# Performance work log

Hardware: AMD Instinct MI355X
Metric: run time of the kernel (lower is better)

The kernel has to match this reference:

```python
import jax, jax.numpy as jnp
import numpy as np

TAU = 0.7        # init kwarg tau
BIG_NEG = -1.0e9 # matches torch big_neg
B, R = 8192, 4096


def setup_inputs() -> dict:
    key = jax.random.key(0)
    k1, k2 = jax.random.split(key)
    s = jax.random.normal(k1, (B, R), dtype=jnp.float32)
    mask = jax.random.uniform(k2, (B, R), dtype=jnp.float32)  # compared against 0.5
    return {"s": s, "mask": mask, "k": 8}


def reference(s, mask, k):
    # mask-apply then temperature scale
    z = jnp.where(mask > 0.5, s, jnp.full_like(s, BIG_NEG)) / max(TAU, 1e-6)
    # sparsemax along axis 1: sort descending, cumsum, support-size threshold
    z_sorted = -jnp.sort(-z, axis=1)                       # [B, R] descending
    z_cumsum = jnp.cumsum(z_sorted, axis=1)                # [B, R]
    r = jnp.arange(1, R + 1, dtype=z.dtype)[None, :]       # [1, R] ranks 1..R
    cond = 1.0 + r * z_sorted > z_cumsum                   # [B, R] support indicator
    k_sup = jnp.sum(cond, axis=1, keepdims=True)           # [B, 1] int support size
    tau_star = (jnp.take_along_axis(z_cumsum, k_sup - 1, axis=1) - 1.0) / k_sup.astype(z.dtype)
    p = jnp.maximum(z - tau_star, 0.0)                     # sparsemax probs, sum=1
    # scale by budget k and clip to [0, 1]
    return jnp.minimum(jnp.asarray(float(k), z.dtype) * p, 1.0)
```

## Files before the change

### kernel.cpp

```cpp
#include <hip/hip_runtime.h>


#define R_DIM 4096
#define BLOCK 256
#define V4T   4
#define BIG_NEG -1.0e9f
#define INV_TAU (1.0f / 0.7f)

typedef float fx4 __attribute__((ext_vector_type(4)));

__global__ __launch_bounds__(BLOCK, 4)
void gate_sparsemax_k_kernel(const float* __restrict__ s,
                             const float* __restrict__ m,
                             const int*  __restrict__ kptr,
                             float* __restrict__ out)
{
    __shared__ float red_sum[2][4];
    __shared__ float red_cnt[2][4];
    __shared__ float red_max[4];

    const int tid  = (int)threadIdx.x;
    const int lane = tid & 63;
    const int wid  = tid >> 6;
    const int row  = (int)blockIdx.x;

    const float kf = (float)(*kptr);

    const size_t base = (size_t)row * R_DIM;
    const fx4* sv4 = (const fx4*)(s + base);
    const fx4* mv4 = (const fx4*)(m + base);
    fx4*       ov4 = (fx4*)(out + base);

    fx4 sv[V4T], mv[V4T];
    #pragma unroll
    for (int t = 0; t < V4T; ++t) sv[t] = __builtin_nontemporal_load(&sv4[t * BLOCK + tid]);
    #pragma unroll
    for (int t = 0; t < V4T; ++t) mv[t] = __builtin_nontemporal_load(&mv4[t * BLOCK + tid]);
    __builtin_amdgcn_sched_barrier(0);

    fx4 zz[V4T];
    float zmax = -3.4028235e38f;
    #pragma unroll
    for (int t = 0; t < V4T; ++t) {
        fx4 zv;
        zv.x = (mv[t].x > 0.5f ? sv[t].x : BIG_NEG) * INV_TAU;
        zv.y = (mv[t].y > 0.5f ? sv[t].y : BIG_NEG) * INV_TAU;
        zv.z = (mv[t].z > 0.5f ? sv[t].z : BIG_NEG) * INV_TAU;
        zv.w = (mv[t].w > 0.5f ? sv[t].w : BIG_NEG) * INV_TAU;
        zz[t] = zv;
        zmax = fmaxf(zmax, fmaxf(fmaxf(zv.x, zv.y), fmaxf(zv.z, zv.w)));
    }

    #pragma unroll
    for (int off = 32; off >= 1; off >>= 1)
        zmax = fmaxf(zmax, __shfl_xor(zmax, off, 64));
    if (lane == 0) red_max[wid] = zmax;
    __syncthreads();
    zmax = fmaxf(fmaxf(red_max[0], red_max[1]), fmaxf(red_max[2], red_max[3]));

    float tau = zmax - 1.0f;
    for (int it = 0; it < 50; ++it) {
        float ssum = 0.0f, cnt = 0.0f;
        #pragma unroll
        for (int t = 0; t < V4T; ++t) {
            const fx4 zv = zz[t];
            if (zv.x > tau) { ssum += zv.x; cnt += 1.0f; }
            if (zv.y > tau) { ssum += zv.y; cnt += 1.0f; }
            if (zv.z > tau) { ssum += zv.z; cnt += 1.0f; }
            if (zv.w > tau) { ssum += zv.w; cnt += 1.0f; }
        }
        #pragma unroll
        for (int off = 32; off >= 1; off >>= 1) {
            ssum += __shfl_xor(ssum, off, 64);
            cnt  += __shfl_xor(cnt,  off, 64);
        }
        const int p = it & 1;
        if (lane == 0) { red_sum[p][wid] = ssum; red_cnt[p][wid] = cnt; }
        __syncthreads();
        const float S = ((red_sum[p][0] + red_sum[p][1]) + (red_sum[p][2] + red_sum[p][3]));
        const float C = ((red_cnt[p][0] + red_cnt[p][1]) + (red_cnt[p][2] + red_cnt[p][3]));
        const float tnew = (S - 1.0f) / C;
        if (tnew == tau) break;
        tau = tnew;
    }

    #pragma unroll
    for (int t = 0; t < V4T; ++t) {
        const fx4 zv = zz[t];
        fx4 ov;
        ov.x = fminf(kf * fmaxf(zv.x - tau, 0.0f), 1.0f);
        ov.y = fminf(kf * fmaxf(zv.y - tau, 0.0f), 1.0f);
        ov.z = fminf(kf * fmaxf(zv.z - tau, 0.0f), 1.0f);
        ov.w = fminf(kf * fmaxf(zv.w - tau, 0.0f), 1.0f);
        __builtin_nontemporal_store(ov, &ov4[t * BLOCK + tid]);
    }
}

extern "C" void kernel_launch(void* const* d_in, const int* in_sizes, int n_in,
                              void* d_out, int out_size, void* d_ws, size_t ws_size,
                              hipStream_t stream) {
    const float* s = (const float*)d_in[0];
    const float* m = (const float*)d_in[1];
    const int*   k = (const int*)d_in[2];
    float* out = (float*)d_out;

    const int nrows = in_sizes[0] / R_DIM;
    gate_sparsemax_k_kernel<<<nrows, BLOCK, 0, stream>>>(s, m, k, out);
}
```

Measured before the change: 291.4 us.

## Map one row per wavefront to drop block-level barriers in sparsemax iteration

Each 64-lane wavefront now owns a whole row of 4096 elements (16 float4 per lane) instead of a 256-thread block sharing a row, so the max and the per-iteration sum reductions need only wave shuffles, with no shared memory or __syncthreads. The support count is taken with ballot+popcount instead of a float shuffle reduction, and mask loads are split into two halves to limit register pressure. In exchange, register use per thread rises sharply (64 floats of z plus mask staging), which can lower occupancy under the launch bounds and reduce memory-level parallelism in this bandwidth-bound kernel.

```diff
diff --git a/kernel.cpp b/kernel.cpp
--- a/kernel.cpp
+++ b/kernel.cpp
@@ -3,26 +3,34 @@
 
 #define R_DIM 4096
 #define BLOCK 256
-#define V4T   4
+#define RPB   4
+#define NCH   16
 #define BIG_NEG -1.0e9f
 #define INV_TAU (1.0f / 0.7f)
 
 typedef float fx4 __attribute__((ext_vector_type(4)));
 
+__device__ __forceinline__ void gate4(fx4& zv, const fx4 mv, float& zmax)
+{
+    zv.x = (mv.x > 0.5f ? zv.x : BIG_NEG) * INV_TAU;
+    zv.y = (mv.y > 0.5f ? zv.y : BIG_NEG) * INV_TAU;
+    zv.z = (mv.z > 0.5f ? zv.z : BIG_NEG) * INV_TAU;
+    zv.w = (mv.w > 0.5f ? zv.w : BIG_NEG) * INV_TAU;
+    zmax = fmaxf(zmax, fmaxf(fmaxf(zv.x, zv.y), fmaxf(zv.z, zv.w)));
+}
+
 __global__ __launch_bounds__(BLOCK, 4)
 void gate_sparsemax_k_kernel(const float* __restrict__ s,
                              const float* __restrict__ m,
                              const int*  __restrict__ kptr,
-                             float* __restrict__ out)
+                             float* __restrict__ out,
+                             int nrows)
 {
-    __shared__ float red_sum[2][4];
-    __shared__ float red_cnt[2][4];
-    __shared__ float red_max[4];
-
     const int tid  = (int)threadIdx.x;
     const int lane = tid & 63;
     const int wid  = tid >> 6;
-    const int row  = (int)blockIdx.x;
+    const int row  = (int)blockIdx.x * RPB + wid;
+    if (row >= nrows) return;
 
     const float kf = (float)(*kptr);
 
@@ -31,68 +39,69 @@
     const fx4* mv4 = (const fx4*)(m + base);
     fx4*       ov4 = (fx4*)(out + base);
 
-    fx4 sv[V4T], mv[V4T];
+    fx4 zz[NCH];
+    fx4 mm[NCH / 2];
+
     #pragma unroll
-    for (int t = 0; t < V4T; ++t) sv[t] = __builtin_nontemporal_load(&sv4[t * BLOCK + tid]);
+    for (int t = 0; t < NCH; ++t)
+        zz[t] = __builtin_nontemporal_load(&sv4[t * 64 + lane]);
     #pragma unroll
-    for (int t = 0; t < V4T; ++t) mv[t] = __builtin_nontemporal_load(&mv4[t * BLOCK + tid]);
+    for (int t = 0; t < NCH / 2; ++t)
+        mm[t] = __builtin_nontemporal_load(&mv4[t * 64 + lane]);
     __builtin_amdgcn_sched_barrier(0);
 
-    fx4 zz[V4T];
     float zmax = -3.4028235e38f;
     #pragma unroll
-    for (int t = 0; t < V4T; ++t) {
-        fx4 zv;
-        zv.x = (mv[t].x > 0.5f ? sv[t].x : BIG_NEG) * INV_TAU;
-        zv.y = (mv[t].y > 0.5f ? sv[t].y : BIG_NEG) * INV_TAU;
-        zv.z = (mv[t].z > 0.5f ? sv[t].z : BIG_NEG) * INV_TAU;
-        zv.w = (mv[t].w > 0.5f ? sv[t].w : BIG_NEG) * INV_TAU;
-        zz[t] = zv;
-        zmax = fmaxf(zmax, fmaxf(fmaxf(zv.x, zv.y), fmaxf(zv.z, zv.w)));
-    }
+    for (int t = 0; t < NCH / 2; ++t)
+        gate4(zz[t], mm[t], zmax);
+
+    #pragma unroll
+    for (int t = 0; t < NCH / 2; ++t)
+        mm[t] = __builtin_nontemporal_load(&mv4[(NCH / 2 + t) * 64 + lane]);
+    __builtin_amdgcn_sched_barrier(0);
+    #pragma unroll
+    for (int t = 0; t < NCH / 2; ++t)
+        gate4(zz[NCH / 2 + t], mm[t], zmax);
 
     #pragma unroll
     for (int off = 32; off >= 1; off >>= 1)
         zmax = fmaxf(zmax, __shfl_xor(zmax, off, 64));
-    if (lane == 0) red_max[wid] = zmax;
-    __syncthreads();
-    zmax = fmaxf(fmaxf(red_max[0], red_max[1]), fmaxf(red_max[2], red_max[3]));
 
     float tau = zmax - 1.0f;
     for (int it = 0; it < 50; ++it) {
-        float ssum = 0.0f, cnt = 0.0f;
+        float ssum = 0.0f;
+        int cnt = 0;
         #pragma unroll
-        for (int t = 0; t < V4T; ++t) {
+        for (int t = 0; t < NCH; ++t) {
             const fx4 zv = zz[t];
-            if (zv.x > tau) { ssum += zv.x; cnt += 1.0f; }
-            if (zv.y > tau) { ssum += zv.y; cnt += 1.0f; }
-            if (zv.z > tau) { ssum += zv.z; cnt += 1.0f; }
-            if (zv.w > tau) { ssum += zv.w; cnt += 1.0f; }
+            ssum += (zv.x > tau) ? zv.x : 0.0f;
+            cnt  += (int)__popcll(__ballot(zv.x > tau));
+            ssum += (zv.y > tau) ? zv.y : 0.0f;
+            cnt  += (int)__popcll(__ballot(zv.y > tau));
+            ssum += (zv.z > tau) ? zv.z : 0.0f;
+            cnt  += (int)__popcll(__ballot(zv.z > tau));
+            ssum += (zv.w > tau) ? zv.w : 0.0f;
+            cnt  += (int)__popcll(__ballot(zv.w > tau));
         }
         #pragma unroll
-        for (int off = 32; off >= 1; off >>= 1) {
+        for (int off = 32; off >= 1; off >>= 1)
             ssum += __shfl_xor(ssum, off, 64);
-            cnt  += __shfl_xor(cnt,  off, 64);
-        }
-        const int p = it & 1;
-        if (lane == 0) { red_sum[p][wid] = ssum; red_cnt[p][wid] = cnt; }
-        __syncthreads();
-        const float S = ((red_sum[p][0] + red_sum[p][1]) + (red_sum[p][2] + red_sum[p][3]));
-        const float C = ((red_cnt[p][0] + red_cnt[p][1]) + (red_cnt[p][2] + red_cnt[p][3]));
-        const float tnew = (S - 1.0f) / C;
+
+        const float C    = (float)cnt;
+        const float tnew = (ssum - 1.0f) / C;
         if (tnew == tau) break;
         tau = tnew;
     }
 
     #pragma unroll
-    for (int t = 0; t < V4T; ++t) {
+    for (int t = 0; t < NCH; ++t) {
         const fx4 zv = zz[t];
         fx4 ov;
         ov.x = fminf(kf * fmaxf(zv.x - tau, 0.0f), 1.0f);
         ov.y = fminf(kf * fmaxf(zv.y - tau, 0.0f), 1.0f);
         ov.z = fminf(kf * fmaxf(zv.z - tau, 0.0f), 1.0f);
         ov.w = fminf(kf * fmaxf(zv.w - tau, 0.0f), 1.0f);
-        __builtin_nontemporal_store(ov, &ov4[t * BLOCK + tid]);
+        __builtin_nontemporal_store(ov, &ov4[t * 64 + lane]);
     }
 }
 
@@ -104,6 +113,7 @@
     const int*   k = (const int*)d_in[2];
     float* out = (float*)d_out;
 
-    const int nrows = in_sizes[0] / R_DIM;
-    gate_sparsemax_k_kernel<<<nrows, BLOCK, 0, stream>>>(s, m, k, out);
+    const int nrows  = in_sizes[0] / R_DIM;
+    const int nblk   = (nrows + RPB - 1) / RPB;
+    gate_sparsemax_k_kernel<<<nblk, BLOCK, 0, stream>>>(s, m, k, out, nrows);
 }
```

Result: slower. 311.5 us (+6.9%).

## Compact sparsemax candidates into LDS and iterate threshold on the small set

Applied to the files above, without the earlier changes.

Elements above zmax-1 are gathered into a shared-memory candidate buffer with atomics. When the buffer holds at most 128 values, the fixed-point threshold iteration runs redundantly per thread over that small set, with no block-wide reductions or barriers per iteration. If the buffer overflows, the code falls back to the original full-row reduction loop. Occupancy hint is raised to 6 blocks per SM. The per-element LDS atomics add contention, and every thread reading the buffer serially adds latency.

```diff
diff --git a/kernel.cpp b/kernel.cpp
--- a/kernel.cpp
+++ b/kernel.cpp
@@ -4,20 +4,23 @@
 #define R_DIM 4096
 #define BLOCK 256
 #define V4T   4
+#define CAP   128
 #define BIG_NEG -1.0e9f
 #define INV_TAU (1.0f / 0.7f)
 
 typedef float fx4 __attribute__((ext_vector_type(4)));
 
-__global__ __launch_bounds__(BLOCK, 4)
+__global__ __launch_bounds__(BLOCK, 6)
 void gate_sparsemax_k_kernel(const float* __restrict__ s,
                              const float* __restrict__ m,
                              const int*  __restrict__ kptr,
                              float* __restrict__ out)
 {
+    __shared__ float red_max[4];
+    __shared__ float cand[CAP];
+    __shared__ int   ccnt;
     __shared__ float red_sum[2][4];
     __shared__ float red_cnt[2][4];
-    __shared__ float red_max[4];
 
     const int tid  = (int)threadIdx.x;
     const int lane = tid & 63;
@@ -30,6 +33,8 @@
     const fx4* sv4 = (const fx4*)(s + base);
     const fx4* mv4 = (const fx4*)(m + base);
     fx4*       ov4 = (fx4*)(out + base);
+
+    if (tid == 0) ccnt = 0;
 
     fx4 sv[V4T], mv[V4T];
     #pragma unroll
@@ -58,30 +63,55 @@
     __syncthreads();
     zmax = fmaxf(fmaxf(red_max[0], red_max[1]), fmaxf(red_max[2], red_max[3]));
 
-    float tau = zmax - 1.0f;
-    for (int it = 0; it < 50; ++it) {
-        float ssum = 0.0f, cnt = 0.0f;
-        #pragma unroll
-        for (int t = 0; t < V4T; ++t) {
-            const fx4 zv = zz[t];
-            if (zv.x > tau) { ssum += zv.x; cnt += 1.0f; }
-            if (zv.y > tau) { ssum += zv.y; cnt += 1.0f; }
-            if (zv.z > tau) { ssum += zv.z; cnt += 1.0f; }
-            if (zv.w > tau) { ssum += zv.w; cnt += 1.0f; }
+    const float thr = zmax - 1.0f;
+    #pragma unroll
+    for (int t = 0; t < V4T; ++t) {
+        const fx4 zv = zz[t];
+        if (zv.x > thr) { int i = atomicAdd(&ccnt, 1); if (i < CAP) cand[i] = zv.x; }
+        if (zv.y > thr) { int i = atomicAdd(&ccnt, 1); if (i < CAP) cand[i] = zv.y; }
+        if (zv.z > thr) { int i = atomicAdd(&ccnt, 1); if (i < CAP) cand[i] = zv.z; }
+        if (zv.w > thr) { int i = atomicAdd(&ccnt, 1); if (i < CAP) cand[i] = zv.w; }
+    }
+    __syncthreads();
+    const int ncand = ccnt;
+
+    float tau = thr;
+    if (ncand <= CAP) {
+        for (int it = 0; it < 50; ++it) {
+            float S = 0.0f; int C = 0;
+            for (int i = 0; i < ncand; ++i) {
+                const float c = cand[i];
+                if (c > tau) { S += c; ++C; }
+            }
+            const float tnew = (S - 1.0f) / (float)C;
+            if (tnew == tau) break;
+            tau = tnew;
         }
-        #pragma unroll
-        for (int off = 32; off >= 1; off >>= 1) {
-            ssum += __shfl_xor(ssum, off, 64);
-            cnt  += __shfl_xor(cnt,  off, 64);
+    } else {
+        for (int it = 0; it < 50; ++it) {
+            float ssum = 0.0f, cnt = 0.0f;
+            #pragma unroll
+            for (int t = 0; t < V4T; ++t) {
+                const fx4 zv = zz[t];
+                if (zv.x > tau) { ssum += zv.x; cnt += 1.0f; }
+                if (zv.y > tau) { ssum += zv.y; cnt += 1.0f; }
+                if (zv.z > tau) { ssum += zv.z; cnt += 1.0f; }
+                if (zv.w > tau) { ssum += zv.w; cnt += 1.0f; }
+            }
+            #pragma unroll
+            for (int off = 32; off >= 1; off >>= 1) {
+                ssum += __shfl_xor(ssum, off, 64);
+                cnt  += __shfl_xor(cnt,  off, 64);
+            }
+            const int p = it & 1;
+            if (lane == 0) { red_sum[p][wid] = ssum; red_cnt[p][wid] = cnt; }
+            __syncthreads();
+            const float S = ((red_sum[p][0] + red_sum[p][1]) + (red_sum[p][2] + red_sum[p][3]));
+            const float C = ((red_cnt[p][0] + red_cnt[p][1]) + (red_cnt[p][2] + red_cnt[p][3]));
+            const float tnew = (S - 1.0f) / C;
+            if (tnew == tau) break;
+            tau = tnew;
         }
-        const int p = it & 1;
-        if (lane == 0) { red_sum[p][wid] = ssum; red_cnt[p][wid] = cnt; }
-        __syncthreads();
-        const float S = ((red_sum[p][0] + red_sum[p][1]) + (red_sum[p][2] + red_sum[p][3]));
-        const float C = ((red_cnt[p][0] + red_cnt[p][1]) + (red_cnt[p][2] + red_cnt[p][3]));
-        const float tnew = (S - 1.0f) / C;
-        if (tnew == tau) break;
-        tau = tnew;
     }
 
     #pragma unroll
```

Result: no change. 295.0 us (+1.2%).
